# Kernel tuning notes

Measured on AMD Instinct MI355X. Metric: run time of the kernel, lower is better.

## Reference

```python
import jax, jax.numpy as jnp
import numpy as np

N_E = 1024
E_DIM = 256
BETA = 0.25
EPS = 1e-10


def setup_inputs() -> dict:
    key = jax.random.key(0)
    k1, k2 = jax.random.split(key)
    z = jax.random.normal(k1, (32, E_DIM, 32, 32), dtype=jnp.float32)
    emb = jax.random.normal(k2, (N_E, E_DIM), dtype=jnp.float32)
    return {"z": z, "emb": emb}


def reference(z, emb):
    sg = jax.lax.stop_gradient
    # (B, C, H, W) -> (B, H, W, C)
    zp = jnp.transpose(z, (0, 2, 3, 1))
    zf = zp.reshape(-1, E_DIM)  # (N, C), N = B*H*W
    # squared euclidean distances: ||z||^2 + ||e||^2 - 2 z e^T  -> (N, n_e)
    d = (jnp.sum(zf * zf, axis=1, keepdims=True)
         + jnp.sum(emb * emb, axis=1)
         - 2.0 * jnp.matmul(zf, emb.T))
    idx = jnp.argmin(d, axis=1)  # (N,)
    # one-hot @ codebook == gather (same math, no dense one-hot matmul)
    z_q1 = emb[idx].reshape(zp.shape)  # (B, H, W, C)
    # loss: note original does NOT detach z_q1 anywhere
    loss = jnp.mean((z_q1 - zp) ** 2) + BETA * jnp.mean((z_q1 - sg(zp)) ** 2)
    # straight-through (original detaches z, not z_q1)
    z_q = zp + (z_q1 - sg(zp))
    # perplexity from mean one-hot encodings = normalized histogram of indices
    counts = jnp.bincount(idx, length=N_E)
    e_mean = counts.astype(zf.dtype) / idx.shape[0]
    perplexity = jnp.exp(-jnp.sum(e_mean * jnp.log(e_mean + EPS)))
    z_q = jnp.transpose(z_q, (0, 3, 1, 2))
    z_q1_out = jnp.transpose(z_q1, (0, 3, 1, 2))
    return loss, z_q, perplexity, idx, z_q1_out
```

## Files before the change

kernel.cpp:

```cpp
#include <hip/hip_runtime.h>
#include <hip/hip_bf16.h>
#include <math.h>

#define CDIM 256
#define HW   1024
#define NVEC 32768
#define NE   1024
#define ZSIZE 8388608
#define NSPLIT 2
#define MARGIN 0.05f

#define OUT_LOSS 0
#define OUT_ZQ   1
#define OUT_PERP 8388609
#define OUT_IDX  8388610
#define OUT_ZQ1  8421378

#define WS_LOSS   0
#define WS_RCNT   64
#define WS_HIST   128
#define WS_ENORM  4224
#define WS_IDX    8448
#define WS_RLIST  139520
#define WS_S1     270592
#define WS_S2     532736
#define WS_J1     794880
#define WS_EBH    1057024
#define WS_EBL    1581312
#define WS_ZBH    2105600
#define WS_ZBL    18882816

typedef __attribute__((ext_vector_type(8))) short short8;
typedef __attribute__((ext_vector_type(4))) float f32x4;
typedef __attribute__((ext_vector_type(8))) unsigned short ushort8v;

__device__ __forceinline__ unsigned short bf16_rne(float x) {
    union { float f; unsigned u; } v; v.f = x;
    unsigned r = v.u + 0x7FFFu + ((v.u >> 16) & 1u);
    return (unsigned short)(r >> 16);
}
__device__ __forceinline__ float bf16_to_f(unsigned short h) {
    union { unsigned u; float f; } v; v.u = ((unsigned)h) << 16;
    return v.f;
}
__device__ __forceinline__ void lds_barrier() {
    asm volatile("s_waitcnt lgkmcnt(0)\n\ts_barrier" ::: "memory");
}

__global__ __launch_bounds__(256) void vq_prep(
    const float* __restrict__ z, const float* __restrict__ emb,
    unsigned short* __restrict__ zbh, unsigned short* __restrict__ zbl,
    unsigned short* __restrict__ ebh, unsigned short* __restrict__ ebl,
    float* __restrict__ enorm)
{
    const int tid = threadIdx.x, w = tid >> 6, L = tid & 63;
    if (blockIdx.x < 512) {
        __shared__ unsigned short th[64 * 264];
        __shared__ unsigned short tl[64 * 264];
        const int b = blockIdx.x >> 4, hw0 = (blockIdx.x & 15) << 6;
        const float* zp = z + (size_t)b * (CDIM * HW) + hw0;
        for (int i = 0; i < 16; ++i) {
            int k = (i * 4 + w) * 4;
            float f0 = zp[(size_t)(k + 0) * HW + L];
            float f1 = zp[(size_t)(k + 1) * HW + L];
            float f2 = zp[(size_t)(k + 2) * HW + L];
            float f3 = zp[(size_t)(k + 3) * HW + L];
            ushort4 hi = { bf16_rne(f0), bf16_rne(f1), bf16_rne(f2), bf16_rne(f3) };
            ushort4 lo = { bf16_rne(f0 - bf16_to_f(hi.x)), bf16_rne(f1 - bf16_to_f(hi.y)),
                           bf16_rne(f2 - bf16_to_f(hi.z)), bf16_rne(f3 - bf16_to_f(hi.w)) };
            *(ushort4*)&th[L * 264 + k] = hi;
            *(ushort4*)&tl[L * 264 + k] = lo;
        }
        __syncthreads();
#pragma unroll
        for (int it = 0; it < 8; ++it) {
            int row = it * 8 + (tid >> 5);
            int kc = (tid & 31) * 8;
            size_t o = (size_t)(b * 1024 + hw0 + row) * CDIM + kc;
            *(ushort8v*)(zbh + o) = *(ushort8v*)&th[row * 264 + kc];
            *(ushort8v*)(zbl + o) = *(ushort8v*)&tl[row * 264 + kc];
        }
    } else {
        const int cb = (int)(blockIdx.x - 512) * 64;
        for (int p = 0; p < 16; ++p) {
            int code = cb + p * 4 + w;
            float4 v = *(const float4*)(emb + (size_t)code * CDIM + L * 4);
            float s = v.x * v.x + v.y * v.y + v.z * v.z + v.w * v.w;
            for (int off = 32; off; off >>= 1) s += __shfl_down(s, off, 64);
            if (L == 0) enorm[code] = s;
            ushort4 hi = { bf16_rne(v.x), bf16_rne(v.y), bf16_rne(v.z), bf16_rne(v.w) };
            ushort4 lo = { bf16_rne(v.x - bf16_to_f(hi.x)), bf16_rne(v.y - bf16_to_f(hi.y)),
                           bf16_rne(v.z - bf16_to_f(hi.z)), bf16_rne(v.w - bf16_to_f(hi.w)) };
            *(ushort4*)(ebh + (size_t)code * CDIM + L * 4) = hi;
            *(ushort4*)(ebl + (size_t)code * CDIM + L * 4) = lo;
        }
    }
}

__global__ __launch_bounds__(256, 2) void vq_mfma3(
    const unsigned short* __restrict__ zbh, const unsigned short* __restrict__ zbl,
    const unsigned short* __restrict__ ebh, const unsigned short* __restrict__ ebl,
    const float* __restrict__ enorm,
    float* __restrict__ s1_ws, float* __restrict__ s2_ws, int* __restrict__ j1_ws)
{
    __shared__ short albuf[32768];
    __shared__ short bbuf[8192];

    const int tid = threadIdx.x, w = tid >> 6, L = tid & 63;
    const int l15 = L & 15, q = L >> 4;
    const int r16 = tid & 15, ch = (tid >> 4) & 3;
    const int mtile = blockIdx.x & 255, js = blockIdx.x >> 8;
    const int n0 = mtile << 7;
    const int jsbase = js << 9;

#pragma unroll
    for (int ro = 0; ro < 16; ++ro) {
        const int seg = ro * 4 + w;
        const int sw2 = seg >> 4, smf = (seg >> 3) & 1, skk = seg & 7;
        short8 v = *(const short8*)(zbl + (size_t)(n0 + sw2 * 32 + smf * 16 + r16) * CDIM + skk * 32 + ch * 8);
        *(short8*)(albuf + seg * 512 + L * 8) = v;
    }
    short8 AH[2][8];
#pragma unroll
    for (int mf = 0; mf < 2; ++mf)
#pragma unroll
        for (int kk = 0; kk < 8; ++kk)
            AH[mf][kk] = *(const short8*)(zbh + (size_t)(n0 + w * 32 + mf * 16 + l15) * CDIM + kk * 32 + q * 8);
    __syncthreads();

    float s1[2][4], s2[2][4]; int j1[2][4];
#pragma unroll
    for (int mf = 0; mf < 2; ++mf)
#pragma unroll
        for (int r = 0; r < 4; ++r) { s1[mf][r] = -3.4e38f; s2[mf][r] = -3.4e38f; j1[mf][r] = 0; }

    for (int j0i = 0; j0i < 4; ++j0i) {
        const int j0 = jsbase + j0i * 128;
        f32x4 acc[2][8] = {};
        short8 st[4];
#pragma unroll
        for (int ro = 0; ro < 4; ++ro) {
            const unsigned short* src = (ro >= 2) ? ebl : ebh;
            const int jf = (ro & 1) * 4 + w;
            st[ro] = *(const short8*)(src + (size_t)(j0 + jf * 16 + r16) * CDIM + ch * 8);
        }
#pragma unroll
        for (int kk = 0; kk < 8; ++kk) {
            lds_barrier();
#pragma unroll
            for (int ro = 0; ro < 4; ++ro)
                *(short8*)(bbuf + (ro * 4 + w) * 512 + L * 8) = st[ro];
            if (kk < 7) {
                const int k0n = (kk + 1) * 32;
#pragma unroll
                for (int ro = 0; ro < 4; ++ro) {
                    const unsigned short* src = (ro >= 2) ? ebl : ebh;
                    const int jf = (ro & 1) * 4 + w;
                    st[ro] = *(const short8*)(src + (size_t)(j0 + jf * 16 + r16) * CDIM + k0n + ch * 8);
                }
            }
            lds_barrier();
            short8 AL0 = *(const short8*)(albuf + (w * 16 + kk) * 512 + L * 8);
            short8 AL1 = *(const short8*)(albuf + (w * 16 + 8 + kk) * 512 + L * 8);
#pragma unroll
            for (int jf = 0; jf < 8; ++jf) {
                short8 Bh = *(const short8*)(bbuf + jf * 512 + L * 8);
                short8 Bl = *(const short8*)(bbuf + (8 + jf) * 512 + L * 8);
                acc[0][jf] = __builtin_amdgcn_mfma_f32_16x16x32_bf16(AH[0][kk], Bh, acc[0][jf], 0, 0, 0);
                acc[1][jf] = __builtin_amdgcn_mfma_f32_16x16x32_bf16(AH[1][kk], Bh, acc[1][jf], 0, 0, 0);
                acc[0][jf] = __builtin_amdgcn_mfma_f32_16x16x32_bf16(AH[0][kk], Bl, acc[0][jf], 0, 0, 0);
                acc[1][jf] = __builtin_amdgcn_mfma_f32_16x16x32_bf16(AH[1][kk], Bl, acc[1][jf], 0, 0, 0);
                acc[0][jf] = __builtin_amdgcn_mfma_f32_16x16x32_bf16(AL0, Bh, acc[0][jf], 0, 0, 0);
                acc[1][jf] = __builtin_amdgcn_mfma_f32_16x16x32_bf16(AL1, Bh, acc[1][jf], 0, 0, 0);
            }
        }
#pragma unroll
        for (int jf = 0; jf < 8; ++jf) {
            const int j = j0 + jf * 16 + l15;
            const float hn = 0.5f * enorm[j];
#pragma unroll
            for (int mf = 0; mf < 2; ++mf)
#pragma unroll
                for (int r = 0; r < 4; ++r) {
                    float s = acc[mf][jf][r] - hn;
                    if (s > s1[mf][r]) { s2[mf][r] = s1[mf][r]; s1[mf][r] = s; j1[mf][r] = j; }
                    else if (s > s2[mf][r]) s2[mf][r] = s;
                }
        }
    }

#pragma unroll
    for (int mf = 0; mf < 2; ++mf)
#pragma unroll
        for (int r = 0; r < 4; ++r) {
            float a1 = s1[mf][r], a2 = s2[mf][r]; int aj = j1[mf][r];
            for (int m = 1; m < 16; m <<= 1) {
                float o1 = __shfl_xor(a1, m, 64);
                float o2 = __shfl_xor(a2, m, 64);
                int   oj = __shfl_xor(aj, m, 64);
                if (o1 > a1 || (o1 == a1 && oj < aj)) { a2 = fmaxf(a1, o2); a1 = o1; aj = oj; }
                else a2 = fmaxf(a2, o1);
            }
            if (l15 == 0) {
                int o = js * NVEC + n0 + w * 32 + mf * 16 + q * 4 + r;
                s1_ws[o] = a1; s2_ws[o] = a2; j1_ws[o] = aj;
            }
        }
}

__global__ __launch_bounds__(256) void vq_merge(
    const float* __restrict__ s1_ws, const float* __restrict__ s2_ws,
    const int* __restrict__ j1_ws, int* __restrict__ idx_ws,
    float* __restrict__ idx_out, int* __restrict__ hist,
    int* __restrict__ rcnt, int* __restrict__ rlist)
{
    int n = blockIdx.x * 256 + threadIdx.x;
    float b1 = -3.4e38f, b2 = -3.4e38f; int bj = 0;
#pragma unroll
    for (int s = 0; s < NSPLIT; ++s) {
        float a1 = s1_ws[s * NVEC + n], a2 = s2_ws[s * NVEC + n];
        int aj = j1_ws[s * NVEC + n];
        if (a1 > b1 || (a1 == b1 && aj < bj)) { b2 = fmaxf(b1, a2); b1 = a1; bj = aj; }
        else b2 = fmaxf(b2, a1);
    }
    idx_ws[n] = bj;
    if (b1 - b2 < MARGIN) {
        int p = atomicAdd(rcnt, 1); rlist[p] = n;
    } else {
        idx_out[n] = (float)bj;
        atomicAdd(&hist[bj], 1);
    }
}

__global__ __launch_bounds__(256) void vq_rescue(
    const float* __restrict__ z, const float* __restrict__ emb,
    const float* __restrict__ enorm, const int* __restrict__ rcnt,
    const int* __restrict__ rlist, int* __restrict__ idx_ws,
    float* __restrict__ idx_out, int* __restrict__ hist)
{
    __shared__ __align__(16) float zrow[256];
    __shared__ float rs[4];
    __shared__ int   rj[4];
    const int tid = threadIdx.x;
    const int wv = tid >> 6, L = tid & 63;
    const int count = *rcnt;

    for (int it = blockIdx.x; it < count; it += gridDim.x) {
        __syncthreads();
        const int n = rlist[it];
        zrow[tid] = z[(size_t)(n >> 10) * (CDIM * HW) + (size_t)tid * HW + (n & 1023)];
        __syncthreads();
        const float4 zv = *(const float4*)&zrow[L * 4];

        float b1 = -3.4e38f; int bj = 0x7fffffff;
        const int jbase = wv << 8;
        const int jodd = L >> 5;
#pragma unroll 4
        for (int jo = 0; jo < 256; jo += 2) {
            const int jA = jbase + jo;
            const float4 eA = *(const float4*)(emb + (size_t)jA * CDIM + L * 4);
            const float4 eB = *(const float4*)(emb + (size_t)(jA + 1) * CDIM + L * 4);
            float pA = fmaf(zv.x, eA.x, fmaf(zv.y, eA.y, fmaf(zv.z, eA.z, zv.w * eA.w)));
            float pB = fmaf(zv.x, eB.x, fmaf(zv.y, eB.y, fmaf(zv.z, eB.z, zv.w * eB.w)));
            float tA = pA + __shfl_xor(pA, 32, 64);
            float tB = pB + __shfl_xor(pB, 32, 64);
            float u = (L < 32) ? tA : tB;
            u += __shfl_xor(u, 16, 64);
            u += __shfl_xor(u, 8, 64);
            u += __shfl_xor(u, 4, 64);
            u += __shfl_xor(u, 2, 64);
            u += __shfl_xor(u, 1, 64);
            const int j = jA + jodd;
            const float s = u - 0.5f * enorm[j];
            if (s > b1 || (s == b1 && j < bj)) { b1 = s; bj = j; }
        }
        {
            const float o1 = __shfl_xor(b1, 32, 64);
            const int   oj = __shfl_xor(bj, 32, 64);
            if (o1 > b1 || (o1 == b1 && oj < bj)) { b1 = o1; bj = oj; }
        }
        if (L == 0) { rs[wv] = b1; rj[wv] = bj; }
        __syncthreads();
        if (tid == 0) {
            float f1 = rs[0]; int fj = rj[0];
#pragma unroll
            for (int v = 1; v < 4; ++v)
                if (rs[v] > f1 || (rs[v] == f1 && rj[v] < fj)) { f1 = rs[v]; fj = rj[v]; }
            idx_ws[n] = fj;
            idx_out[n] = (float)fj;
            atomicAdd(&hist[fj], 1);
        }
    }
}

__global__ __launch_bounds__(256) void vq_gather(
    const float* __restrict__ z, const float* __restrict__ emb,
    const int* __restrict__ idx_ws, float* __restrict__ zq,
    float* __restrict__ zq1, double* __restrict__ loss_sum)
{
    __shared__ float es[32 * 129];
    __shared__ int ids[32];
    __shared__ float wred[4];

    const int tid = threadIdx.x, w = tid >> 6, L = tid & 63;
    const int b   = blockIdx.x >> 6;
    const int half = (blockIdx.x >> 5) & 1;
    const int hw0 = (blockIdx.x & 31) << 5;
    const int n0  = (b << 10) + hw0;
    const int c0  = half << 7;

    if (tid < 32) ids[tid] = idx_ws[n0 + tid];
    __syncthreads();

#pragma unroll
    for (int p = 0; p < 4; ++p) {
        int u = p * 256 + tid;
        int r = u >> 5, cq = (u & 31) * 4;
        float4 v = *(const float4*)(emb + (size_t)ids[r] * CDIM + c0 + cq);
        es[r * 129 + cq + 0] = v.x;
        es[r * 129 + cq + 1] = v.y;
        es[r * 129 + cq + 2] = v.z;
        es[r * 129 + cq + 3] = v.w;
    }
    __syncthreads();

    const int row = L & 31, cp = L >> 5;
    const size_t zbase = (size_t)b * (CDIM * HW) + hw0 + row;
    float ls = 0.f;
    for (int rd = 0; rd < 16; ++rd) {
        int cl = rd * 8 + w * 2 + cp;
        size_t off = zbase + (size_t)(c0 + cl) * HW;
        float zv = z[off];
        float e  = es[row * 129 + cl];
        float d  = e - zv;
        zq[off]  = zv + d;
        zq1[off] = e;
        ls += d * d;
    }

    for (int off = 32; off; off >>= 1) ls += __shfl_down(ls, off, 64);
    if (L == 0) wred[w] = ls;
    __syncthreads();
    if (tid == 0)
        atomicAdd(loss_sum, (double)(wred[0] + wred[1] + wred[2] + wred[3]));
}

__global__ __launch_bounds__(1024) void vq_final(
    const int* __restrict__ hist, const double* __restrict__ loss_sum,
    float* __restrict__ out_loss, float* __restrict__ out_perp)
{
    int tid = threadIdx.x;
    float em = (float)hist[tid] * (1.0f / 32768.0f);
    float term = em * logf(em + 1e-10f);
    for (int off = 32; off; off >>= 1) term += __shfl_down(term, off, 64);
    __shared__ float red[16];
    int lane = tid & 63, wv = tid >> 6;
    if (lane == 0) red[wv] = term;
    __syncthreads();
    if (tid == 0) {
        float s = 0.f;
        for (int i = 0; i < 16; ++i) s += red[i];
        *out_perp = expf(-s);
        *out_loss = (float)(*loss_sum * 1.25 / 8388608.0);
    }
}

extern "C" void kernel_launch(void* const* d_in, const int* in_sizes, int n_in,
                              void* d_out, int out_size, void* d_ws, size_t ws_size,
                              hipStream_t stream) {
    const float* z   = (const float*)d_in[0];
    const float* emb = (const float*)d_in[1];
    float* out = (float*)d_out;
    char*  ws  = (char*)d_ws;

    double* loss_sum    = (double*)(ws + WS_LOSS);
    int*    rcnt        = (int*)(ws + WS_RCNT);
    int*    hist        = (int*)(ws + WS_HIST);
    float*  enorm       = (float*)(ws + WS_ENORM);
    int*    idx_ws      = (int*)(ws + WS_IDX);
    int*    rlist       = (int*)(ws + WS_RLIST);
    float*  s1_ws       = (float*)(ws + WS_S1);
    float*  s2_ws       = (float*)(ws + WS_S2);
    int*    j1_ws       = (int*)(ws + WS_J1);
    unsigned short* ebh = (unsigned short*)(ws + WS_EBH);
    unsigned short* ebl = (unsigned short*)(ws + WS_EBL);
    unsigned short* zbh = (unsigned short*)(ws + WS_ZBH);
    unsigned short* zbl = (unsigned short*)(ws + WS_ZBL);

    hipMemsetAsync(d_ws, 0, 4224, stream);

    vq_prep  <<<528, 256, 0, stream>>>(z, emb, zbh, zbl, ebh, ebl, enorm);
    vq_mfma3 <<<512, 256, 0, stream>>>(zbh, zbl, ebh, ebl, enorm, s1_ws, s2_ws, j1_ws);
    vq_merge <<<128, 256, 0, stream>>>(s1_ws, s2_ws, j1_ws, idx_ws, out + OUT_IDX, hist, rcnt, rlist);
    vq_rescue<<<512, 256, 0, stream>>>(z, emb, enorm, rcnt, rlist, idx_ws, out + OUT_IDX, hist);
    vq_gather<<<2048, 256, 0, stream>>>(z, emb, idx_ws, out + OUT_ZQ, out + OUT_ZQ1, loss_sum);
    vq_final <<<1, 1024, 0, stream>>>(hist, loss_sum, out + OUT_LOSS, out + OUT_PERP);
}
```

Measured before the change: 277.5 us.

## Stage codebook through double-buffered LDS in rescue kernel with register prefetch

The rescue kernel now streams the codebook in 64-row chunks into a double-buffered shared-memory tile, prefetching the next chunk into registers while computing on the current one. Each group of four threads computes one code's dot product over a quarter of the channels, which replaces the long wave-wide shuffle reduction per code with two shuffles. Norms are cached in LDS. This costs about 140KB of LDS per block, which lowers occupancy, and adds barriers per chunk.

```diff
diff --git a/kernel.cpp b/kernel.cpp
--- a/kernel.cpp
+++ b/kernel.cpp
@@ -238,48 +238,86 @@
     const int* __restrict__ rlist, int* __restrict__ idx_ws,
     float* __restrict__ idx_out, int* __restrict__ hist)
 {
-    __shared__ __align__(16) float zrow[256];
+    __shared__ __align__(16) float lds_e[2][64 * 272];
+    __shared__ __align__(16) float zrowp[4 * 68];
+    __shared__ float lds_en[NE];
     __shared__ float rs[4];
     __shared__ int   rj[4];
+
     const int tid = threadIdx.x;
-    const int wv = tid >> 6, L = tid & 63;
+    const int w = tid >> 6, L = tid & 63;
+    const int c = tid >> 2, qp = tid & 3;
+    const int wr = (L >> 4) * 68 + (L & 15) * 4;
     const int count = *rcnt;
+
+    for (int i = tid; i < NE; i += 256) lds_en[i] = enorm[i];
 
     for (int it = blockIdx.x; it < count; it += gridDim.x) {
         __syncthreads();
         const int n = rlist[it];
-        zrow[tid] = z[(size_t)(n >> 10) * (CDIM * HW) + (size_t)tid * HW + (n & 1023)];
-        __syncthreads();
-        const float4 zv = *(const float4*)&zrow[L * 4];
+
+        float4 st[16];
+#pragma unroll
+        for (int i = 0; i < 16; ++i)
+            st[i] = *(const float4*)(emb + (size_t)(i * 4 + w) * CDIM + L * 4);
+        const float zval = z[(size_t)(n >> 10) * (CDIM * HW) + (size_t)tid * HW + (n & 1023)];
+
+        zrowp[(tid >> 6) * 68 + (tid & 63)] = zval;
+#pragma unroll
+        for (int i = 0; i < 16; ++i)
+            *(float4*)&lds_e[0][(i * 4 + w) * 272 + wr] = st[i];
+        lds_barrier();
+
+        float4 zr[16];
+#pragma unroll
+        for (int k = 0; k < 16; ++k)
+            zr[k] = *(const float4*)&zrowp[qp * 68 + k * 4];
 
         float b1 = -3.4e38f; int bj = 0x7fffffff;
-        const int jbase = wv << 8;
-        const int jodd = L >> 5;
-#pragma unroll 4
-        for (int jo = 0; jo < 256; jo += 2) {
-            const int jA = jbase + jo;
-            const float4 eA = *(const float4*)(emb + (size_t)jA * CDIM + L * 4);
-            const float4 eB = *(const float4*)(emb + (size_t)(jA + 1) * CDIM + L * 4);
-            float pA = fmaf(zv.x, eA.x, fmaf(zv.y, eA.y, fmaf(zv.z, eA.z, zv.w * eA.w)));
-            float pB = fmaf(zv.x, eB.x, fmaf(zv.y, eB.y, fmaf(zv.z, eB.z, zv.w * eB.w)));
-            float tA = pA + __shfl_xor(pA, 32, 64);
-            float tB = pB + __shfl_xor(pB, 32, 64);
-            float u = (L < 32) ? tA : tB;
-            u += __shfl_xor(u, 16, 64);
-            u += __shfl_xor(u, 8, 64);
-            u += __shfl_xor(u, 4, 64);
-            u += __shfl_xor(u, 2, 64);
-            u += __shfl_xor(u, 1, 64);
-            const int j = jA + jodd;
-            const float s = u - 0.5f * enorm[j];
-            if (s > b1 || (s == b1 && j < bj)) { b1 = s; bj = j; }
-        }
-        {
-            const float o1 = __shfl_xor(b1, 32, 64);
-            const int   oj = __shfl_xor(bj, 32, 64);
+        const int cbase = c * 272 + qp * 68;
+
+#pragma unroll 1
+        for (int p = 0; p < 16; ++p) {
+            if (p < 15) {
+                const int j0 = (p + 1) * 64;
+#pragma unroll
+                for (int i = 0; i < 16; ++i)
+                    st[i] = *(const float4*)(emb + (size_t)(j0 + i * 4 + w) * CDIM + L * 4);
+            }
+            const float* eb = lds_e[p & 1];
+            float pa = 0.f, pb = 0.f;
+#pragma unroll
+            for (int k = 0; k < 16; k += 2) {
+                float4 e0 = *(const float4*)&eb[cbase + k * 4];
+                float4 e1 = *(const float4*)&eb[cbase + k * 4 + 4];
+                pa = fmaf(zr[k].x, e0.x, fmaf(zr[k].y, e0.y,
+                     fmaf(zr[k].z, e0.z, fmaf(zr[k].w, e0.w, pa))));
+                pb = fmaf(zr[k + 1].x, e1.x, fmaf(zr[k + 1].y, e1.y,
+                     fmaf(zr[k + 1].z, e1.z, fmaf(zr[k + 1].w, e1.w, pb))));
+            }
+            float part = pa + pb;
+            part += __shfl_xor(part, 1, 64);
+            part += __shfl_xor(part, 2, 64);
+            const int j = p * 64 + c;
+            const float s = part - 0.5f * lds_en[j];
+            if (s > b1) { b1 = s; bj = j; }
+
+            lds_barrier();
+            if (p < 15) {
+#pragma unroll
+                for (int i = 0; i < 16; ++i)
+                    *(float4*)&lds_e[(p + 1) & 1][(i * 4 + w) * 272 + wr] = st[i];
+            }
+            lds_barrier();
+        }
+
+#pragma unroll
+        for (int m = 4; m <= 32; m <<= 1) {
+            const float o1 = __shfl_xor(b1, m, 64);
+            const int   oj = __shfl_xor(bj, m, 64);
             if (o1 > b1 || (o1 == b1 && oj < bj)) { b1 = o1; bj = oj; }
         }
-        if (L == 0) { rs[wv] = b1; rj[wv] = bj; }
+        if (L == 0) { rs[w] = b1; rj[w] = bj; }
         __syncthreads();
         if (tid == 0) {
             float f1 = rs[0]; int fj = rj[0];
```

Result: slower. 359.8 us (+29.7%).

## Split rescue codebook search across blocks with packed atomicMax merge

Applied to the files above, without the earlier changes.

The rescue kernel now splits each ambiguous row's 1024-code search into 16 chunks handled by separate blocks. The chunks merge through a 64-bit atomicMax on an order-preserving float key packed with the inverted index. A small finalize kernel then writes the indices and histogram. This targets the serial per-row latency of the old rescue loop, which underused the GPU when few rows needed rescue. In exchange it adds an extra launch, repeats the z row load per chunk, and reuses workspace for the score buffer.

```diff
diff --git a/kernel.cpp b/kernel.cpp
--- a/kernel.cpp
+++ b/kernel.cpp
@@ -29,6 +29,7 @@
 #define WS_EBL    1581312
 #define WS_ZBH    2105600
 #define WS_ZBL    18882816
+#define WS_SCORE  WS_EBH
 
 typedef __attribute__((ext_vector_type(8))) short short8;
 typedef __attribute__((ext_vector_type(4))) float f32x4;
@@ -212,9 +213,11 @@
     const float* __restrict__ s1_ws, const float* __restrict__ s2_ws,
     const int* __restrict__ j1_ws, int* __restrict__ idx_ws,
     float* __restrict__ idx_out, int* __restrict__ hist,
-    int* __restrict__ rcnt, int* __restrict__ rlist)
+    int* __restrict__ rcnt, int* __restrict__ rlist,
+    unsigned long long* __restrict__ score)
 {
     int n = blockIdx.x * 256 + threadIdx.x;
+    score[n] = 0ull;
     float b1 = -3.4e38f, b2 = -3.4e38f; int bj = 0;
 #pragma unroll
     for (int s = 0; s < NSPLIT; ++s) {
@@ -235,29 +238,32 @@
 __global__ __launch_bounds__(256) void vq_rescue(
     const float* __restrict__ z, const float* __restrict__ emb,
     const float* __restrict__ enorm, const int* __restrict__ rcnt,
-    const int* __restrict__ rlist, int* __restrict__ idx_ws,
-    float* __restrict__ idx_out, int* __restrict__ hist)
+    const int* __restrict__ rlist, unsigned long long* __restrict__ score)
 {
     __shared__ __align__(16) float zrow[256];
+    __shared__ float en_s[64];
     __shared__ float rs[4];
     __shared__ int   rj[4];
     const int tid = threadIdx.x;
     const int wv = tid >> 6, L = tid & 63;
+    const int chunk = blockIdx.x & 15;
+    const int jwave = chunk * 64 + wv * 16;
+    const int jodd = L >> 5;
+    const int rstride = gridDim.x >> 4;
     const int count = *rcnt;
 
-    for (int it = blockIdx.x; it < count; it += gridDim.x) {
+    for (int it = blockIdx.x >> 4; it < count; it += rstride) {
         __syncthreads();
         const int n = rlist[it];
         zrow[tid] = z[(size_t)(n >> 10) * (CDIM * HW) + (size_t)tid * HW + (n & 1023)];
+        if (tid < 64) en_s[tid] = enorm[chunk * 64 + tid];
         __syncthreads();
         const float4 zv = *(const float4*)&zrow[L * 4];
 
         float b1 = -3.4e38f; int bj = 0x7fffffff;
-        const int jbase = wv << 8;
-        const int jodd = L >> 5;
-#pragma unroll 4
-        for (int jo = 0; jo < 256; jo += 2) {
-            const int jA = jbase + jo;
+#pragma unroll
+        for (int jo = 0; jo < 16; jo += 2) {
+            const int jA = jwave + jo;
             const float4 eA = *(const float4*)(emb + (size_t)jA * CDIM + L * 4);
             const float4 eB = *(const float4*)(emb + (size_t)(jA + 1) * CDIM + L * 4);
             float pA = fmaf(zv.x, eA.x, fmaf(zv.y, eA.y, fmaf(zv.z, eA.z, zv.w * eA.w)));
@@ -271,8 +277,8 @@
             u += __shfl_xor(u, 2, 64);
             u += __shfl_xor(u, 1, 64);
             const int j = jA + jodd;
-            const float s = u - 0.5f * enorm[j];
-            if (s > b1 || (s == b1 && j < bj)) { b1 = s; bj = j; }
+            const float s = u - 0.5f * en_s[wv * 16 + jo + jodd];
+            if (s > b1) { b1 = s; bj = j; }
         }
         {
             const float o1 = __shfl_xor(b1, 32, 64);
@@ -286,10 +292,27 @@
 #pragma unroll
             for (int v = 1; v < 4; ++v)
                 if (rs[v] > f1 || (rs[v] == f1 && rj[v] < fj)) { f1 = rs[v]; fj = rj[v]; }
-            idx_ws[n] = fj;
-            idx_out[n] = (float)fj;
-            atomicAdd(&hist[fj], 1);
-        }
+            unsigned key = __float_as_uint(f1);
+            key = (key & 0x80000000u) ? ~key : (key | 0x80000000u);
+            unsigned long long packed = ((unsigned long long)key << 32) | (unsigned)(~fj);
+            atomicMax(&score[it], packed);
+        }
+    }
+}
+
+__global__ __launch_bounds__(256) void vq_rfin(
+    const int* __restrict__ rcnt, const int* __restrict__ rlist,
+    const unsigned long long* __restrict__ score, int* __restrict__ idx_ws,
+    float* __restrict__ idx_out, int* __restrict__ hist)
+{
+    const int count = *rcnt;
+    for (int it = blockIdx.x * 256 + threadIdx.x; it < count; it += gridDim.x * 256) {
+        const unsigned long long p = score[it];
+        const int fj = (int)(~(unsigned)p) & (NE - 1);
+        const int n = rlist[it];
+        idx_ws[n] = fj;
+        idx_out[n] = (float)fj;
+        atomicAdd(&hist[fj], 1);
     }
 }
 
@@ -386,13 +409,15 @@
     unsigned short* ebl = (unsigned short*)(ws + WS_EBL);
     unsigned short* zbh = (unsigned short*)(ws + WS_ZBH);
     unsigned short* zbl = (unsigned short*)(ws + WS_ZBL);
+    unsigned long long* score = (unsigned long long*)(ws + WS_SCORE);
 
     hipMemsetAsync(d_ws, 0, 4224, stream);
 
     vq_prep  <<<528, 256, 0, stream>>>(z, emb, zbh, zbl, ebh, ebl, enorm);
     vq_mfma3 <<<512, 256, 0, stream>>>(zbh, zbl, ebh, ebl, enorm, s1_ws, s2_ws, j1_ws);
-    vq_merge <<<128, 256, 0, stream>>>(s1_ws, s2_ws, j1_ws, idx_ws, out + OUT_IDX, hist, rcnt, rlist);
-    vq_rescue<<<512, 256, 0, stream>>>(z, emb, enorm, rcnt, rlist, idx_ws, out + OUT_IDX, hist);
+    vq_merge <<<128, 256, 0, stream>>>(s1_ws, s2_ws, j1_ws, idx_ws, out + OUT_IDX, hist, rcnt, rlist, score);
+    vq_rescue<<<2048, 256, 0, stream>>>(z, emb, enorm, rcnt, rlist, score);
+    vq_rfin  <<<8, 256, 0, stream>>>(rcnt, rlist, score, idx_ws, out + OUT_IDX, hist);
     vq_gather<<<2048, 256, 0, stream>>>(z, emb, idx_ws, out + OUT_ZQ, out + OUT_ZQ1, loss_sum);
     vq_final <<<1, 1024, 0, stream>>>(hist, loss_sum, out + OUT_LOSS, out + OUT_PERP);
 }
```

After: 238.7 us. 1.16x faster.
